# Kernel optimization log

Hardware: AMD Instinct MI355X
Metric: run time of the kernel (lower is better)

Reference implementation:

```python
import jax, jax.numpy as jnp
import numpy as np

T = 2048
HIDDEN = 4096
NQ = 32
NKV = 8
HD = 128
THETA = 10000.0


def setup_inputs() -> dict:
    key = jax.random.key(0)
    ks = jax.random.split(key, 5)
    s = 1.0 / np.sqrt(HIDDEN)
    return {
        "positions": jnp.arange(T, dtype=jnp.int32),
        "hidden_states": jax.random.normal(ks[0], (T, HIDDEN), dtype=jnp.float32),
        "wq": jax.random.normal(ks[1], (HIDDEN, NQ * HD), dtype=jnp.float32) * s,
        "wk": jax.random.normal(ks[2], (HIDDEN, NKV * HD), dtype=jnp.float32) * s,
        "wv": jax.random.normal(ks[3], (HIDDEN, NKV * HD), dtype=jnp.float32) * s,
        "wo": jax.random.normal(ks[4], (NQ * HD, HIDDEN), dtype=jnp.float32) * s,
    }


def _rope_neox(x, positions):
    # x: [T, H, HD]; neox style: split halves, rotate
    half = HD // 2
    inv_freq = 1.0 / (THETA ** (jnp.arange(0, half, dtype=jnp.float32) / half))
    ang = positions.astype(jnp.float32)[:, None] * inv_freq[None, :]  # [T, half]
    cos = jnp.cos(ang)[:, None, :]  # [T, 1, half]
    sin = jnp.sin(ang)[:, None, :]
    x1, x2 = x[..., :half], x[..., half:]
    return jnp.concatenate([x1 * cos - x2 * sin, x2 * cos + x1 * sin], axis=-1)


def reference(positions, hidden_states, wq, wk, wv, wo):
    scale = HD ** -0.5
    q = (hidden_states @ wq).reshape(T, NQ, HD)
    k = (hidden_states @ wk).reshape(T, NKV, HD)
    v = (hidden_states @ wv).reshape(T, NKV, HD)
    q = _rope_neox(q, positions)
    k = _rope_neox(k, positions)
    # GQA: repeat kv heads to match q heads
    group = NQ // NKV
    k_r = jnp.repeat(k, group, axis=1)  # [T, NQ, HD]
    v_r = jnp.repeat(v, group, axis=1)
    scores = jnp.einsum('qhd,khd->hqk', q, k_r) * scale  # [NQ, T, T]
    causal = positions[:, None] >= positions[None, :]  # [T, T]
    scores = jnp.where(causal[None, :, :], scores, -jnp.inf)
    probs = jax.nn.softmax(scores, axis=-1)
    attn = jnp.einsum('hqk,khd->qhd', probs, v_r).reshape(T, NQ * HD)
    return attn @ wo
```

## Files before the change

### kernel.cpp

```cpp
#include <hip/hip_runtime.h>

#define T_SEQ  2048
#define HID    4096
#define NQH    32
#define NKVH   8
#define HDIM   128

typedef float  f32x4  __attribute__((ext_vector_type(4)));
typedef __bf16 bf16x8 __attribute__((ext_vector_type(8)));

__device__ __forceinline__ float bf2f(unsigned short u) {
  union { unsigned int i; float f; } v; v.i = ((unsigned int)u) << 16; return v.f;
}
__device__ __forceinline__ unsigned short f2bf(float f) {
  union { float f; unsigned int i; } v; v.f = f;
  unsigned int r = v.i + 0x7fffu + ((v.i >> 16) & 1u);
  return (unsigned short)(r >> 16);
}

__device__ __forceinline__ f32x4 mfma_bf16(bf16x8 a, bf16x8 b, f32x4 c) {
  return __builtin_amdgcn_mfma_f32_16x16x32_bf16(a, b, c, 0, 0, 0);
}

#define GLOAD16(g, l)                                              \
  __builtin_amdgcn_global_load_lds(                                \
      (const __attribute__((address_space(1))) void*)(g),          \
      (__attribute__((address_space(3))) void*)(l), 16, 0, 0)

__global__ void prep_all(const float* __restrict__ hs, unsigned short* __restrict__ hb,
                         const float* __restrict__ wq, unsigned short* __restrict__ wqt,
                         const float* __restrict__ wk, const float* __restrict__ wv,
                         unsigned short* __restrict__ wkvt) {
  __shared__ float tile[64][65];
  const int b = blockIdx.x;
  if (b < 8192) {
    long long i = ((long long)b * 256 + threadIdx.x) * 4;
    float4 v = *(const float4*)(hs + i);
    union { unsigned short u[4]; uint2 p; } o;
    o.u[0] = f2bf(v.x); o.u[1] = f2bf(v.y); o.u[2] = f2bf(v.z); o.u[3] = f2bf(v.w);
    *(uint2*)(hb + i) = o.p;
    return;
  }
  const float* W;
  unsigned short* dst;
  int N, n0, k0;
  if (b < 12288) {
    int bid = b - 8192;  W = wq;  dst = wqt;  N = 4096;
    n0 = (bid & 63) * 64; k0 = (bid >> 6) * 64;
  } else if (b < 13312) {
    int bid = b - 12288; W = wk;  dst = wkvt; N = 1024;
    n0 = (bid & 15) * 64; k0 = (bid >> 4) * 64;
  } else {
    int bid = b - 13312; W = wv;  dst = wkvt + (size_t)1024 * HID; N = 1024;
    n0 = (bid & 15) * 64; k0 = (bid >> 4) * 64;
  }
  int tx = threadIdx.x & 15, ty = threadIdx.x >> 4;
#pragma unroll
  for (int i = 0; i < 4; i++) {
    int k = ty + 16 * i;
    float4 f = *(const float4*)(W + (long long)(k0 + k) * N + n0 + tx * 4);
    tile[tx * 4 + 0][k] = f.x;
    tile[tx * 4 + 1][k] = f.y;
    tile[tx * 4 + 2][k] = f.z;
    tile[tx * 4 + 3][k] = f.w;
  }
  __syncthreads();
#pragma unroll
  for (int i = 0; i < 4; i++) {
    int n = ty + 16 * i;
    union { unsigned short u[4]; uint2 p; } o;
    o.u[0] = f2bf(tile[n][tx * 4 + 0]);
    o.u[1] = f2bf(tile[n][tx * 4 + 1]);
    o.u[2] = f2bf(tile[n][tx * 4 + 2]);
    o.u[3] = f2bf(tile[n][tx * 4 + 3]);
    *(uint2*)(dst + (long long)(n0 + n) * HID + k0 + tx * 4) = o.p;
  }
}

__global__ void transpose_conv(const float* __restrict__ W,
                               unsigned short* __restrict__ Wt, int K, int N) {
  __shared__ float tile[64][65];
  int n0 = blockIdx.x * 64, k0 = blockIdx.y * 64;
  int tx = threadIdx.x & 15, ty = threadIdx.x >> 4;
#pragma unroll
  for (int i = 0; i < 4; i++) {
    int k = ty + 16 * i;
    float4 f = *(const float4*)(W + (long long)(k0 + k) * N + n0 + tx * 4);
    tile[tx * 4 + 0][k] = f.x;
    tile[tx * 4 + 1][k] = f.y;
    tile[tx * 4 + 2][k] = f.z;
    tile[tx * 4 + 3][k] = f.w;
  }
  __syncthreads();
#pragma unroll
  for (int i = 0; i < 4; i++) {
    int n = ty + 16 * i;
    union { unsigned short u[4]; uint2 p; } o;
    o.u[0] = f2bf(tile[n][tx * 4 + 0]);
    o.u[1] = f2bf(tile[n][tx * 4 + 1]);
    o.u[2] = f2bf(tile[n][tx * 4 + 2]);
    o.u[3] = f2bf(tile[n][tx * 4 + 3]);
    *(uint2*)(Wt + (long long)(n0 + n) * K + k0 + tx * 4) = o.p;
  }
}

template <int EPI>
__global__ __launch_bounds__(256) void gemm_bt(const unsigned short* __restrict__ A,
                                               const unsigned short* __restrict__ Bt,
                                               void* __restrict__ Cv,
                                               int M, int N, int K) {
  __shared__ unsigned short As[128 * 64];
  __shared__ unsigned short Bs[128 * 64];
  const int lin = blockIdx.y * gridDim.x + blockIdx.x;
  const int cpx = (gridDim.x * gridDim.y) >> 3;
  const int swz = (lin & 7) * cpx + (lin >> 3);
  const int bx = swz % gridDim.x, by = swz / gridDim.x;

  const int t = threadIdx.x;
  const int lane = t & 63, w = t >> 6;
  const int wr = w >> 1, wc = w & 1;
  const int l15 = lane & 15, lg = lane >> 4;
  const int m0 = by * 128, n0 = bx * 128;

  f32x4 acc[4][4];
#pragma unroll
  for (int i = 0; i < 4; i++)
#pragma unroll
    for (int j = 0; j < 4; j++) acc[i][j] = (f32x4){0.f, 0.f, 0.f, 0.f};

  for (int kt = 0; kt < K; kt += 64) {
    __syncthreads();
#pragma unroll
    for (int s = 0; s < 4; s++) {
      int c = t + s * 256;
      int row = c >> 3, sub = c & 7;
      GLOAD16(A + (long long)(m0 + row) * K + kt + ((sub ^ (row & 7)) * 8),
              (char*)As + (w * 64 + s * 256) * 16);
      GLOAD16(Bt + (long long)(n0 + row) * K + kt + ((sub ^ (row & 7)) * 8),
              (char*)Bs + (w * 64 + s * 256) * 16);
    }
    __syncthreads();

#pragma unroll
    for (int kk = 0; kk < 2; kk++) {
      bf16x8 af[4], bfr[4];
#pragma unroll
      for (int mi = 0; mi < 4; mi++) {
        int row = wr * 64 + mi * 16 + l15;
        af[mi] = *(const bf16x8*)(As + row * 64 + (((kk * 4 + lg) ^ (row & 7)) * 8));
      }
#pragma unroll
      for (int ni = 0; ni < 4; ni++) {
        int row = wc * 64 + ni * 16 + l15;
        bfr[ni] = *(const bf16x8*)(Bs + row * 64 + (((kk * 4 + lg) ^ (row & 7)) * 8));
      }
#pragma unroll
      for (int mi = 0; mi < 4; mi++)
#pragma unroll
        for (int ni = 0; ni < 4; ni++)
          acc[mi][ni] = mfma_bf16(af[mi], bfr[ni], acc[mi][ni]);
    }
  }

  const int row0 = m0 + wr * 64, col0 = n0 + wc * 64;
#pragma unroll
  for (int mi = 0; mi < 4; mi++)
#pragma unroll
    for (int ni = 0; ni < 4; ni++) {
      int rbase = row0 + mi * 16 + lg * 4;
      int col = col0 + ni * 16 + l15;
#pragma unroll
      for (int r = 0; r < 4; r++) {
        float v = acc[mi][ni][r];
        if (EPI == 0)
          ((unsigned short*)Cv)[(long long)(rbase + r) * N + col] = f2bf(v);
        else
          ((float*)Cv)[(long long)(rbase + r) * N + col] = v;
      }
    }
}

__global__ __launch_bounds__(256) void gemm_kv64(const unsigned short* __restrict__ A,
                                                 const unsigned short* __restrict__ Bt,
                                                 unsigned short* __restrict__ Ckv,
                                                 unsigned short* __restrict__ Cvt) {
  __shared__ unsigned short As[64 * 64];
  __shared__ unsigned short Bs[128 * 64];
  __shared__ unsigned short Tt[128 * 64];
  const int lin = blockIdx.y * gridDim.x + blockIdx.x;
  const int swz = (lin & 7) * 64 + (lin >> 3);
  const int bx = swz & 15, by = swz >> 4;

  const int t = threadIdx.x;
  const int lane = t & 63, w = t >> 6;
  const int wr = w >> 1, wc = w & 1;
  const int l15 = lane & 15, lg = lane >> 4;
  const int m0 = by * 64, n0 = bx * 128;
  const int K = HID;

  f32x4 acc[2][4];
#pragma unroll
  for (int i = 0; i < 2; i++)
#pragma unroll
    for (int j = 0; j < 4; j++) acc[i][j] = (f32x4){0.f, 0.f, 0.f, 0.f};

  for (int kt = 0; kt < K; kt += 64) {
    __syncthreads();
#pragma unroll
    for (int s = 0; s < 2; s++) {
      int c = t + s * 256;
      int row = c >> 3, sub = c & 7;
      GLOAD16(A + (long long)(m0 + row) * K + kt + ((sub ^ (row & 7)) * 8),
              (char*)As + (w * 64 + s * 256) * 16);
    }
#pragma unroll
    for (int s = 0; s < 4; s++) {
      int c = t + s * 256;
      int row = c >> 3, sub = c & 7;
      GLOAD16(Bt + (long long)(n0 + row) * K + kt + ((sub ^ (row & 7)) * 8),
              (char*)Bs + (w * 64 + s * 256) * 16);
    }
    __syncthreads();

#pragma unroll
    for (int kk = 0; kk < 2; kk++) {
      bf16x8 af[2], bfr[4];
#pragma unroll
      for (int mi = 0; mi < 2; mi++) {
        int row = wr * 32 + mi * 16 + l15;
        af[mi] = *(const bf16x8*)(As + row * 64 + (((kk * 4 + lg) ^ (row & 7)) * 8));
      }
#pragma unroll
      for (int ni = 0; ni < 4; ni++) {
        int row = wc * 64 + ni * 16 + l15;
        bfr[ni] = *(const bf16x8*)(Bs + row * 64 + (((kk * 4 + lg) ^ (row & 7)) * 8));
      }
#pragma unroll
      for (int mi = 0; mi < 2; mi++)
#pragma unroll
        for (int ni = 0; ni < 4; ni++)
          acc[mi][ni] = mfma_bf16(af[mi], bfr[ni], acc[mi][ni]);
    }
  }

  const int row0 = m0 + wr * 32, col0 = n0 + wc * 64;
  if (n0 < 1024) {
#pragma unroll
    for (int mi = 0; mi < 2; mi++)
#pragma unroll
      for (int ni = 0; ni < 4; ni++) {
        int rbase = row0 + mi * 16 + lg * 4;
        int col = col0 + ni * 16 + l15;
#pragma unroll
        for (int r = 0; r < 4; r++)
          Ckv[(long long)(rbase + r) * 1024 + col] = f2bf(acc[mi][ni][r]);
      }
  } else {
#pragma unroll
    for (int mi = 0; mi < 2; mi++)
#pragma unroll
      for (int ni = 0; ni < 4; ni++) {
        int nloc = wc * 64 + ni * 16 + l15;
#pragma unroll
        for (int r = 0; r < 4; r++) {
          int mloc = wr * 32 + mi * 16 + lg * 4 + r;
          Tt[nloc * 64 + (mloc ^ ((nloc & 7) << 3))] = f2bf(acc[mi][ni][r]);
        }
      }
    __syncthreads();
    const int nloc = t >> 1;
#pragma unroll
    for (int cc = 0; cc < 8; cc++) {
      int ci = (t & 1) * 8 + cc;
      uint2 v = *(const uint2*)(Tt + nloc * 64 +
                                (((ci >> 1) ^ (nloc & 7)) * 8 + (ci & 1) * 4));
      int nc = (ci >> 3) * 8 + 2 * (ci & 3) + ((ci >> 2) & 1);
      *(uint2*)(Cvt + (long long)(n0 - 1024 + nloc) * T_SEQ + m0 + nc * 4) = v;
    }
  }
}

__global__ void rope_all(unsigned short* __restrict__ qb,
                         unsigned short* __restrict__ kb,
                         const int* __restrict__ positions,
                         int* __restrict__ cnt) {
  if (blockIdx.x == 0 && threadIdx.x < 8) cnt[threadIdx.x] = 0;
  const int w = threadIdx.x >> 6, d = threadIdx.x & 63;
  const int gid = blockIdx.x * 4 + w;
  unsigned short* row;
  int t;
  bool isq;
  if (gid < T_SEQ * NQH) {
    int h = gid & (NQH - 1); t = gid >> 5;
    row = qb + (size_t)t * (NQH * HDIM) + (size_t)h * HDIM;
    isq = true;
  } else {
    int g = gid - T_SEQ * NQH;
    int h = g & (NKVH - 1); t = g >> 3;
    row = kb + (size_t)t * (NKVH * HDIM) + (size_t)h * HDIM;
    isq = false;
  }
  double inv = exp2(-(double)d * 0.20762050593046014);
  double ang = (double)positions[t] * inv;
  double c = cos(ang), s = sin(ang);
  if (isq) { c *= 0.12751744416986895; s *= 0.12751744416986895; }
  float x1 = bf2f(row[d]), x2 = bf2f(row[d + 64]);
  row[d]      = f2bf((float)((double)x1 * c - (double)x2 * s));
  row[d + 64] = f2bf((float)((double)x2 * c + (double)x1 * s));
}

__global__ __launch_bounds__(256) void attn_kernel(const unsigned short* __restrict__ qb,
                                                   const unsigned short* __restrict__ kb,
                                                   const unsigned short* __restrict__ vt,
                                                   unsigned short* __restrict__ ab,
                                                   int* __restrict__ cnt) {
  __shared__ unsigned short Ks[2][64 * 128];
  __shared__ unsigned short Vs[2][128 * 64];
  __shared__ int s_item;

  const int xcd = blockIdx.x & 7;
  const int kvh = xcd;
  const int t = threadIdx.x, lane = t & 63, w = t >> 6;
  const int l15 = lane & 15, lg = lane >> 4;

  auto stage = [&](int kts, int bsel) {
#pragma unroll
    for (int s = 0; s < 4; s++) {
      int c = t + s * 256;
      int row = c >> 4, chk = c & 15;
      GLOAD16(kb + (long long)(kts * 64 + row) * (NKVH * HDIM) + kvh * HDIM +
                  ((chk ^ (row & 7)) * 8),
              (char*)(&Ks[bsel][0]) + (w * 64 + s * 256) * 16);
    }
#pragma unroll
    for (int s = 0; s < 4; s++) {
      int c = t + s * 256;
      int row = c >> 3, chk = c & 7;
      GLOAD16(vt + (long long)(kvh * HDIM + row) * T_SEQ + kts * 64 +
                  ((chk ^ (row & 7)) * 8),
              (char*)(&Vs[bsel][0]) + (w * 64 + s * 256) * 16);
    }
  };

  for (;;) {
    __syncthreads();
    if (t == 0) s_item = atomicAdd(&cnt[xcd], 1);
    __syncthreads();
    const int item = s_item;
    if (item >= 128) break;
    const int j = 31 - (item >> 2);
    const int head = xcd * 4 + (item & 3);
    const int q0 = j * 64;

    bf16x8 qf[4];
#pragma unroll
    for (int kk = 0; kk < 4; kk++)
      qf[kk] = *(const bf16x8*)(qb + (long long)(q0 + w * 16 + l15) * (NQH * HDIM) +
                                head * HDIM + kk * 32 + lg * 8);

    f32x4 accO[8];
#pragma unroll
    for (int db = 0; db < 8; db++) accO[db] = (f32x4){0.f, 0.f, 0.f, 0.f};
    float mrun = -3e38f, lrun = 0.f;

    stage(0, 0);
    for (int kt = 0; kt <= j; kt++) {
      const int cur = kt & 1;
      __syncthreads();
      if (kt < j) stage(kt + 1, cur ^ 1);

      f32x4 accS[4];
#pragma unroll
      for (int kc = 0; kc < 4; kc++) accS[kc] = (f32x4){0.f, 0.f, 0.f, 0.f};
      __builtin_amdgcn_s_setprio(1);
#pragma unroll
      for (int kk = 0; kk < 4; kk++)
#pragma unroll
        for (int kc = 0; kc < 4; kc++) {
          int row = kc * 16 + l15;
          bf16x8 a = *(const bf16x8*)(&Ks[cur][0] + row * 128 + (((kk * 4 + lg) ^ (l15 & 7)) * 8));
          accS[kc] = mfma_bf16(a, qf[kk], accS[kc]);
        }
      __builtin_amdgcn_s_setprio(0);

      float pm[4][4];
      if (kt == j) {
        const int qloc = w * 16 + l15;
#pragma unroll
        for (int kc = 0; kc < 4; kc++)
#pragma unroll
          for (int r = 0; r < 4; r++)
            pm[kc][r] = (kc * 16 + lg * 4 + r > qloc) ? -3e38f : accS[kc][r];
      } else {
#pragma unroll
        for (int kc = 0; kc < 4; kc++)
#pragma unroll
          for (int r = 0; r < 4; r++) pm[kc][r] = accS[kc][r];
      }

      float rm = pm[0][0];
#pragma unroll
      for (int kc = 0; kc < 4; kc++)
#pragma unroll
        for (int r = 0; r < 4; r++) rm = fmaxf(rm, pm[kc][r]);
      if (__any(rm > mrun + 8.f)) {
        rm = fmaxf(rm, __shfl_xor(rm, 16, 64));
        rm = fmaxf(rm, __shfl_xor(rm, 32, 64));
        float mn = fmaxf(mrun, rm);
        float corr = exp2f(mrun - mn);
        mrun = mn;
        lrun *= corr;
        float cO[4];
#pragma unroll
        for (int r = 0; r < 4; r++) cO[r] = __shfl(corr, lg * 4 + r, 64);
#pragma unroll
        for (int db = 0; db < 8; db++)
#pragma unroll
          for (int r = 0; r < 4; r++) accO[db][r] *= cO[r];
      }

      float p[4][4];
#pragma unroll
      for (int kc = 0; kc < 4; kc++)
#pragma unroll
        for (int r = 0; r < 4; r++) {
          p[kc][r] = exp2f(pm[kc][r] - mrun);
          lrun += p[kc][r];
        }
      bf16x8 pa0, pa1;
#pragma unroll
      for (int jj = 0; jj < 8; jj++) {
        pa0[jj] = (__bf16)p[(jj >> 2)][jj & 3];
        pa1[jj] = (__bf16)p[2 + (jj >> 2)][jj & 3];
      }

      __builtin_amdgcn_s_setprio(1);
#pragma unroll
      for (int db = 0; db < 8; db++) {
        int vrow = db * 16 + l15;
        bf16x8 b = *(const bf16x8*)(&Vs[cur][0] + vrow * 64 + ((lg ^ (vrow & 7)) * 8));
        accO[db] = mfma_bf16(pa0, b, accO[db]);
      }
#pragma unroll
      for (int db = 0; db < 8; db++) {
        int vrow = db * 16 + l15;
        bf16x8 b = *(const bf16x8*)(&Vs[cur][0] + vrow * 64 + (((4 + lg) ^ (vrow & 7)) * 8));
        accO[db] = mfma_bf16(pa1, b, accO[db]);
      }
      __builtin_amdgcn_s_setprio(0);
    }

    lrun += __shfl_xor(lrun, 16, 64);
    lrun += __shfl_xor(lrun, 32, 64);
    float lO[4];
#pragma unroll
    for (int r = 0; r < 4; r++) lO[r] = __shfl(lrun, lg * 4 + r, 64);
#pragma unroll
    for (int db = 0; db < 8; db++)
#pragma unroll
      for (int r = 0; r < 4; r++) {
        int qr = q0 + w * 16 + lg * 4 + r;
        int col = head * HDIM + db * 16 + l15;
        ((__bf16*)ab)[(long long)qr * (NQH * HDIM) + col] = (__bf16)(accO[db][r] / lO[r]);
      }
  }
}

extern "C" void kernel_launch(void* const* d_in, const int* in_sizes, int n_in,
                              void* d_out, int out_size, void* d_ws, size_t ws_size,
                              hipStream_t stream) {
  const int*   positions = (const int*)d_in[0];
  const float* hs = (const float*)d_in[1];
  const float* wq = (const float*)d_in[2];
  const float* wk = (const float*)d_in[3];
  const float* wv = (const float*)d_in[4];
  const float* wo = (const float*)d_in[5];
  float* out = (float*)d_out;

  const size_t SZ_WQT = (size_t)HID * HID * 2;
  const size_t SZ_WKV = (size_t)2048 * HID * 2;
  const size_t SZ_HB  = (size_t)T_SEQ * HID * 2;
  const size_t SZ_QB  = (size_t)T_SEQ * NQH * HDIM * 2;
  const size_t SZ_KB  = (size_t)T_SEQ * NKVH * HDIM * 2;
  const size_t need = SZ_WQT + SZ_WKV + SZ_HB + SZ_QB + SZ_KB * 2 + 64;
  if (ws_size < need) return;

  char* p = (char*)d_ws;
  unsigned short* wqt  = (unsigned short*)p; p += SZ_WQT;
  unsigned short* wkvt = (unsigned short*)p; p += SZ_WKV;
  unsigned short* hb   = (unsigned short*)p; p += SZ_HB;
  unsigned short* qb   = (unsigned short*)p; p += SZ_QB;
  unsigned short* kb   = (unsigned short*)p; p += SZ_KB;
  unsigned short* vtb  = (unsigned short*)p; p += SZ_KB;
  int* cnt = (int*)p;
  unsigned short* ab   = hb;

  prep_all<<<14336, 256, 0, stream>>>(hs, hb, wq, wqt, wk, wv, wkvt);

  gemm_bt<0><<<dim3((NQH * HDIM) / 128, T_SEQ / 128), 256, 0, stream>>>(hb, wqt, qb, T_SEQ, NQH * HDIM, HID);
  gemm_kv64<<<dim3(16, 32), 256, 0, stream>>>(hb, wkvt, kb, vtb);

  rope_all<<<(T_SEQ * (NQH + NKVH)) / 4, 256, 0, stream>>>(qb, kb, positions, cnt);

  attn_kernel<<<512, 256, 0, stream>>>(qb, kb, vtb, ab, cnt);

  transpose_conv<<<dim3(HID / 64, (NQH * HDIM) / 64), 256, 0, stream>>>(wo, wqt, NQH * HDIM, HID);
  gemm_bt<2><<<dim3(HID / 128, T_SEQ / 128), 256, 0, stream>>>(ab, wqt, out, T_SEQ, HID, NQH * HDIM);
}
```

Before: 357.5 us.

## Split-K the Q and output projections into two bf16 partials

Replaces the single-pass Q and O projection GEMMs with a split-K kernel that runs two K-halves as separate z-blocks, doubling the grid from 512 to 1024 blocks. Each half writes a bf16 partial into a scratch buffer. For Q the two partials are summed inside the RoPE kernel, and for O a new reduce kernel adds them into the fp32 output. This raises parallelism and CU occupancy, at the cost of extra partial-buffer traffic, an added launch, and extra bf16 rounding of the partial sums.

```diff
diff --git a/kernel.cpp b/kernel.cpp
--- a/kernel.cpp
+++ b/kernel.cpp
@@ -104,13 +104,16 @@
   }
 }
 
-template <int EPI>
-__global__ __launch_bounds__(256) void gemm_bt(const unsigned short* __restrict__ A,
+__global__ __launch_bounds__(256) void gemm_sk(const unsigned short* __restrict__ A,
                                                const unsigned short* __restrict__ Bt,
-                                               void* __restrict__ Cv,
-                                               int M, int N, int K) {
+                                               unsigned short* __restrict__ P0,
+                                               unsigned short* __restrict__ P1) {
   __shared__ unsigned short As[128 * 64];
   __shared__ unsigned short Bs[128 * 64];
+  const int K = HID;
+  const int kbeg = blockIdx.z * (HID / 2), kend = kbeg + (HID / 2);
+  unsigned short* P = blockIdx.z ? P1 : P0;
+
   const int lin = blockIdx.y * gridDim.x + blockIdx.x;
   const int cpx = (gridDim.x * gridDim.y) >> 3;
   const int swz = (lin & 7) * cpx + (lin >> 3);
@@ -128,7 +131,7 @@
 #pragma unroll
     for (int j = 0; j < 4; j++) acc[i][j] = (f32x4){0.f, 0.f, 0.f, 0.f};
 
-  for (int kt = 0; kt < K; kt += 64) {
+  for (int kt = kbeg; kt < kend; kt += 64) {
     __syncthreads();
 #pragma unroll
     for (int s = 0; s < 4; s++) {
@@ -170,13 +173,8 @@
       int rbase = row0 + mi * 16 + lg * 4;
       int col = col0 + ni * 16 + l15;
 #pragma unroll
-      for (int r = 0; r < 4; r++) {
-        float v = acc[mi][ni][r];
-        if (EPI == 0)
-          ((unsigned short*)Cv)[(long long)(rbase + r) * N + col] = f2bf(v);
-        else
-          ((float*)Cv)[(long long)(rbase + r) * N + col] = v;
-      }
+      for (int r = 0; r < 4; r++)
+        P[(long long)(rbase + r) * 4096 + col] = f2bf(acc[mi][ni][r]);
     }
 }
 
@@ -281,32 +279,50 @@
 }
 
 __global__ void rope_all(unsigned short* __restrict__ qb,
+                         const unsigned short* __restrict__ qp1,
                          unsigned short* __restrict__ kb,
                          const int* __restrict__ positions,
                          int* __restrict__ cnt) {
   if (blockIdx.x == 0 && threadIdx.x < 8) cnt[threadIdx.x] = 0;
   const int w = threadIdx.x >> 6, d = threadIdx.x & 63;
   const int gid = blockIdx.x * 4 + w;
-  unsigned short* row;
   int t;
-  bool isq;
+  double inv = exp2(-(double)d * 0.20762050593046014);
   if (gid < T_SEQ * NQH) {
     int h = gid & (NQH - 1); t = gid >> 5;
-    row = qb + (size_t)t * (NQH * HDIM) + (size_t)h * HDIM;
-    isq = true;
+    size_t off = (size_t)t * (NQH * HDIM) + (size_t)h * HDIM;
+    unsigned short* row = qb + off;
+    const unsigned short* row1 = qp1 + off;
+    double ang = (double)positions[t] * inv;
+    double c = cos(ang) * 0.12751744416986895, s = sin(ang) * 0.12751744416986895;
+    float x1 = bf2f(row[d]) + bf2f(row1[d]);
+    float x2 = bf2f(row[d + 64]) + bf2f(row1[d + 64]);
+    row[d]      = f2bf((float)((double)x1 * c - (double)x2 * s));
+    row[d + 64] = f2bf((float)((double)x2 * c + (double)x1 * s));
   } else {
     int g = gid - T_SEQ * NQH;
     int h = g & (NKVH - 1); t = g >> 3;
-    row = kb + (size_t)t * (NKVH * HDIM) + (size_t)h * HDIM;
-    isq = false;
-  }
-  double inv = exp2(-(double)d * 0.20762050593046014);
-  double ang = (double)positions[t] * inv;
-  double c = cos(ang), s = sin(ang);
-  if (isq) { c *= 0.12751744416986895; s *= 0.12751744416986895; }
-  float x1 = bf2f(row[d]), x2 = bf2f(row[d + 64]);
-  row[d]      = f2bf((float)((double)x1 * c - (double)x2 * s));
-  row[d + 64] = f2bf((float)((double)x2 * c + (double)x1 * s));
+    unsigned short* row = kb + (size_t)t * (NKVH * HDIM) + (size_t)h * HDIM;
+    double ang = (double)positions[t] * inv;
+    double c = cos(ang), s = sin(ang);
+    float x1 = bf2f(row[d]), x2 = bf2f(row[d + 64]);
+    row[d]      = f2bf((float)((double)x1 * c - (double)x2 * s));
+    row[d + 64] = f2bf((float)((double)x2 * c + (double)x1 * s));
+  }
+}
+
+__global__ void reduce_o(const unsigned short* __restrict__ p0,
+                         const unsigned short* __restrict__ p1,
+                         float* __restrict__ out) {
+  long long i = ((long long)blockIdx.x * 256 + threadIdx.x) * 4;
+  uint2 a = *(const uint2*)(p0 + i);
+  uint2 b = *(const uint2*)(p1 + i);
+  float4 o;
+  o.x = bf2f((unsigned short)(a.x & 0xffff)) + bf2f((unsigned short)(b.x & 0xffff));
+  o.y = bf2f((unsigned short)(a.x >> 16))    + bf2f((unsigned short)(b.x >> 16));
+  o.z = bf2f((unsigned short)(a.y & 0xffff)) + bf2f((unsigned short)(b.y & 0xffff));
+  o.w = bf2f((unsigned short)(a.y >> 16))    + bf2f((unsigned short)(b.y >> 16));
+  *(float4*)(out + i) = o;
 }
 
 __global__ __launch_bounds__(256) void attn_kernel(const unsigned short* __restrict__ qb,
@@ -494,16 +510,18 @@
   unsigned short* vtb  = (unsigned short*)p; p += SZ_KB;
   int* cnt = (int*)p;
   unsigned short* ab   = hb;
+  unsigned short* qp1  = (unsigned short*)out;
 
   prep_all<<<14336, 256, 0, stream>>>(hs, hb, wq, wqt, wk, wv, wkvt);
 
-  gemm_bt<0><<<dim3((NQH * HDIM) / 128, T_SEQ / 128), 256, 0, stream>>>(hb, wqt, qb, T_SEQ, NQH * HDIM, HID);
+  gemm_sk<<<dim3(32, 16, 2), 256, 0, stream>>>(hb, wqt, qb, qp1);
   gemm_kv64<<<dim3(16, 32), 256, 0, stream>>>(hb, wkvt, kb, vtb);
 
-  rope_all<<<(T_SEQ * (NQH + NKVH)) / 4, 256, 0, stream>>>(qb, kb, positions, cnt);
+  rope_all<<<(T_SEQ * (NQH + NKVH)) / 4, 256, 0, stream>>>(qb, qp1, kb, positions, cnt);
 
   attn_kernel<<<512, 256, 0, stream>>>(qb, kb, vtb, ab, cnt);
 
   transpose_conv<<<dim3(HID / 64, (NQH * HDIM) / 64), 256, 0, stream>>>(wo, wqt, NQH * HDIM, HID);
-  gemm_bt<2><<<dim3(HID / 128, T_SEQ / 128), 256, 0, stream>>>(ab, wqt, out, T_SEQ, HID, NQH * HDIM);
-}
+  gemm_sk<<<dim3(32, 16, 2), 256, 0, stream>>>(ab, wqt, qb, wkvt);
+  reduce_o<<<(T_SEQ * HID) / 1024, 256, 0, stream>>>(qb, wkvt, out);
+}
```

After: 403.0 us. 12.7% more time.
